# Kernel optimization log

Hardware: AMD Instinct MI355X
Metric: run time of the kernel (lower is better)

The kernel has to match this reference:

```python
import jax, jax.numpy as jnp
import numpy as np

V = 1024      # visible_size (channel_size)
H = 2048      # hidden_size
F = V + H     # full_size
T = 64        # timesteps
REC = 0.8     # params['lambda']


def setup_inputs() -> dict:
    key = jax.random.key(0)
    k1, k2, k3 = jax.random.split(key, 3)
    X = jax.random.normal(k1, (T, V), jnp.float32)
    # scale W so tanh does not fully saturate (fan-in scaling, like default init)
    W = jax.random.normal(k2, (F, F), jnp.float32) / np.float32(np.sqrt(F))
    b = jax.random.normal(k3, (F,), jnp.float32) * 0.01
    # Lambda: visible block = REC, hidden block = 1, diagonal of visible block = 1
    lam = jnp.concatenate(
        [jnp.full((V, V), REC, jnp.float32), jnp.ones((V, H), jnp.float32)], axis=1
    )
    lam = lam.at[jnp.arange(V), jnp.arange(V)].set(1.0)
    return {"X": X, "W": W, "b": b, "lam": lam}


def reference(X, W, b, lam):
    v = lam.shape[0]           # visible size
    one_minus_lam_vis = 1.0 - lam[:, :v]  # zero outside visible block anyway

    def step(carry, x_t):
        R, _ = carry
        WR = R @ W.T + b                      # [V, F] Linear applied row-wise
        U = lam * WR                          # gated recurrent part
        # I has x_t broadcast across rows in the visible block, zeros elsewhere
        U = U.at[:, :v].add(one_minus_lam_vis * x_t[None, :])
        R_next = jnp.tanh(U)                  # phi = torch.tanh
        return (R_next, U), None

    R0 = jnp.zeros((v, W.shape[0]), X.dtype)
    (_, U_last), _ = jax.lax.scan(step, (R0, R0), X)
    # torch.diag(U[:, :visible]) -> diagonal entries, shape [V]
    idx = jnp.arange(v)
    return U_last[idx, idx]
```

## Files before the change

kernel.cpp:

```cpp
#include <hip/hip_runtime.h>
#include <math.h>

#define V 1024
#define H 2048
#define F 3072
#define T 64
#define REC 0.8f

#define BM 128
#define BN 128
#define KT16 (F / 16)
#define KTW  (KT16 / 4)

typedef _Float16 half8 __attribute__((ext_vector_type(8)));
typedef float floatx16 __attribute__((ext_vector_type(16)));

__device__ __forceinline__ float fast_tanh(float u) {
    float e = __expf(2.f * u);
    return 1.f - 2.f * __builtin_amdgcn_rcpf(e + 1.f);
}


__global__ __launch_bounds__(256)
void conv_w_fm(const float* __restrict__ W, _Float16* __restrict__ Wfm) {
    const int ct = blockIdx.y;
    const int ix = blockIdx.x * 256 + threadIdx.x;
    const int kt = ix >> 8;
    const int q  = ix & 255;
    const int n  = ct * 128 + ((q >> 6) & 3) * 32 + (q & 31);
    const int k0 = kt * 16 + ((q >> 5) & 1) * 8;
    const float* src = W + (size_t)n * F + k0;
    float4 v0 = *(const float4*)src;
    float4 v1 = *(const float4*)(src + 4);
    half8 o = { (_Float16)v0.x, (_Float16)v0.y, (_Float16)v0.z, (_Float16)v0.w,
                (_Float16)v1.x, (_Float16)v1.y, (_Float16)v1.z, (_Float16)v1.w };
    *(half8*)(Wfm + ((size_t)(ct * KT16 + kt) * 2048 + q * 8)) = o;
}

__global__ __launch_bounds__(256)
void init_step0(const float* __restrict__ b, const float* __restrict__ x0,
                _Float16* __restrict__ Rfm) {
    const int rt = blockIdx.y;
    const int ix = blockIdx.x * 256 + threadIdx.x;
    const int kt = ix >> 8;
    const int q  = ix & 255;
    const int gi = rt * 128 + ((q >> 6) & 3) * 32 + (q & 31);
    const int k0 = kt * 16 + ((q >> 5) & 1) * 8;
    half8 o;
    #pragma unroll
    for (int e = 0; e < 8; ++e) {
        int gj = k0 + e;
        float wr = b[gj];
        float u = (gj >= V || gi == gj) ? wr : (REC * wr + (1.f - REC) * x0[gj]);
        o[e] = (_Float16)fast_tanh(u);
    }
    *(half8*)(Rfm + ((size_t)(rt * KT16 + kt) * 2048 + q * 8)) = o;
}

__global__ __launch_bounds__(512, 2)
void frnn_step(const _Float16* __restrict__ Rin, const _Float16* __restrict__ Wfm,
               const float* __restrict__ b, const float* __restrict__ xt,
               _Float16* __restrict__ Rout, float* __restrict__ out, int is_last)
{
    __shared__ float red[16384];

    const int tid  = threadIdx.x;
    const int lane = tid & 63;
    const int wid  = tid >> 6;
    const int sp   = wid & 1;
    const int kg   = wid >> 1;
    const int row0 = blockIdx.y * BM;
    const int col0 = blockIdx.x * BN;
    const int lane8 = lane * 8;
    const int kg48 = kg * KTW;

    const _Float16* abase = Rin + ((size_t)blockIdx.y * KT16 * 2048
                                   + sp * 1024 + lane8);
    const _Float16* bbase = Wfm + ((size_t)blockIdx.x * KT16 * 2048 + lane8);

    floatx16 acc[2][4];
    #pragma unroll
    for (int i = 0; i < 2; ++i)
        #pragma unroll
        for (int j = 0; j < 4; ++j)
            #pragma unroll
            for (int r = 0; r < 16; ++r) acc[i][j][r] = 0.f;

    half8 fa0[3], fa1[3], fb0[3], fb1[3], fb2[3], fb3[3];

#define LOADK(S, KTI)                                                           \
  {                                                                             \
    const size_t off = (size_t)(kg48 + (KTI)) * 2048;                           \
    const _Float16* ap = abase + off;                                           \
    const _Float16* bp = bbase + off;                                           \
    fa0[S] = *(const half8*)ap;                                                 \
    fa1[S] = *(const half8*)(ap + 512);                                         \
    fb0[S] = *(const half8*)bp;                                                 \
    fb1[S] = *(const half8*)(bp + 512);                                         \
    fb2[S] = *(const half8*)(bp + 1024);                                        \
    fb3[S] = *(const half8*)(bp + 1536);                                        \
  }

    LOADK(0, 0)
    LOADK(1, 1)

#define BODY(S, PFS, JJ)                                                        \
  {                                                                             \
    int pj = (JJ) + 2; if (pj > KTW - 1) pj = KTW - 1;                          \
    LOADK(PFS, pj)                                                              \
    __builtin_amdgcn_s_setprio(1);                                              \
    acc[0][0] = __builtin_amdgcn_mfma_f32_32x32x16_f16(fa0[S], fb0[S], acc[0][0],0,0,0);\
    acc[0][1] = __builtin_amdgcn_mfma_f32_32x32x16_f16(fa0[S], fb1[S], acc[0][1],0,0,0);\
    acc[0][2] = __builtin_amdgcn_mfma_f32_32x32x16_f16(fa0[S], fb2[S], acc[0][2],0,0,0);\
    acc[0][3] = __builtin_amdgcn_mfma_f32_32x32x16_f16(fa0[S], fb3[S], acc[0][3],0,0,0);\
    acc[1][0] = __builtin_amdgcn_mfma_f32_32x32x16_f16(fa1[S], fb0[S], acc[1][0],0,0,0);\
    acc[1][1] = __builtin_amdgcn_mfma_f32_32x32x16_f16(fa1[S], fb1[S], acc[1][1],0,0,0);\
    acc[1][2] = __builtin_amdgcn_mfma_f32_32x32x16_f16(fa1[S], fb2[S], acc[1][2],0,0,0);\
    acc[1][3] = __builtin_amdgcn_mfma_f32_32x32x16_f16(fa1[S], fb3[S], acc[1][3],0,0,0);\
    __builtin_amdgcn_s_setprio(0);                                              \
  }

    #pragma unroll 1
    for (int j3 = 0; j3 < KTW / 3; ++j3) {
        const int JJ = j3 * 3;
        BODY(0, 2, JJ)
        BODY(1, 0, JJ + 1)
        BODY(2, 1, JJ + 2)
    }
#undef BODY
#undef LOADK

    const int m32 = lane & 31, hh = lane >> 5;
    float b_r[4], x_r[4];
    if (kg == 0) {
        #pragma unroll
        for (int j = 0; j < 4; ++j) {
            int gj = col0 + j * 32 + m32;
            b_r[j] = b[gj];
            x_r[j] = (gj < V) ? xt[gj] : 0.f;
        }
    }

    float* red0 = &red[sp * 8192];
    float* red1 = &red[sp * 8192 + 4096];
    #pragma unroll 1
    for (int w = 1; w < 4; ++w) {
        if (kg == w) {
            #pragma unroll
            for (int j = 0; j < 4; ++j)
                #pragma unroll
                for (int q4 = 0; q4 < 4; ++q4) {
                    float4 v0 = { acc[0][j][4*q4],   acc[0][j][4*q4+1],
                                  acc[0][j][4*q4+2], acc[0][j][4*q4+3] };
                    float4 v1 = { acc[1][j][4*q4],   acc[1][j][4*q4+1],
                                  acc[1][j][4*q4+2], acc[1][j][4*q4+3] };
                    *(float4*)(red0 + (j*4 + q4) * 256 + lane * 4) = v0;
                    *(float4*)(red1 + (j*4 + q4) * 256 + lane * 4) = v1;
                }
        }
        __syncthreads();
        if (kg == 0) {
            #pragma unroll
            for (int j = 0; j < 4; ++j)
                #pragma unroll
                for (int q4 = 0; q4 < 4; ++q4) {
                    float4 v0 = *(const float4*)(red0 + (j*4 + q4) * 256 + lane * 4);
                    float4 v1 = *(const float4*)(red1 + (j*4 + q4) * 256 + lane * 4);
                    acc[0][j][4*q4]   += v0.x; acc[0][j][4*q4+1] += v0.y;
                    acc[0][j][4*q4+2] += v0.z; acc[0][j][4*q4+3] += v0.w;
                    acc[1][j][4*q4]   += v1.x; acc[1][j][4*q4+1] += v1.y;
                    acc[1][j][4*q4+2] += v1.z; acc[1][j][4*q4+3] += v1.w;
                }
        }
        __syncthreads();
    }

    if (kg == 0) {
        #pragma unroll
        for (int i = 0; i < 2; ++i) {
            const int mb = sp * 2 + i;
            #pragma unroll
            for (int j = 0; j < 4; ++j) {
                const int gj = col0 + j * 32 + m32;
                const int kt = gj >> 4;
                const int h2 = (gj >> 3) & 1;
                const int e  = gj & 7;
                _Float16* tb = Rout + ((size_t)(blockIdx.y * KT16 + kt) * 2048
                                       + (mb * 2 + h2) * 256 + e);
                const float bj = b_r[j];
                const float xj = x_r[j];
                const bool vis = (gj < V);
                #pragma unroll
                for (int r = 0; r < 16; ++r) {
                    const int mrow = 4 * hh + (r & 3) + 8 * (r >> 2);
                    const int gi = row0 + mb * 32 + mrow;
                    float wr = acc[i][j][r] + bj;
                    float u = (!vis || gi == gj) ? wr : (REC * wr + (1.f - REC) * xj);
                    tb[mrow * 8] = (_Float16)fast_tanh(u);
                    if (is_last && gi == gj) out[gi] = u;
                }
            }
        }
    }
}

extern "C" void kernel_launch(void* const* d_in, const int* in_sizes, int n_in,
                              void* d_out, int out_size, void* d_ws, size_t ws_size,
                              hipStream_t stream) {
    const float* X = (const float*)d_in[0];
    const float* W = (const float*)d_in[1];
    const float* b = (const float*)d_in[2];
    float* out = (float*)d_out;

    _Float16* Wfm = (_Float16*)d_ws;
    _Float16* Ra  = Wfm + (size_t)F * F;
    _Float16* Rb  = Ra + (size_t)V * F;

    conv_w_fm<<<dim3(192, 24), 256, 0, stream>>>(W, Wfm);
    init_step0<<<dim3(192, 8), 256, 0, stream>>>(b, X, Ra);

    for (int t = 1; t < T; ++t) {
        _Float16* Rin  = (t & 1) ? Ra : Rb;
        _Float16* Rout = (t & 1) ? Rb : Ra;
        frnn_step<<<dim3(24, 8), 512, 0, stream>>>(Rin, Wfm, b, X + (size_t)t * V,
                                                   Rout, out, t == T - 1);
    }
}
```

Measured before the change: 2.333 ms.

## Fuse per-timestep launches into persistent cooperative kernel with grid barrier

Replaces the 63 separate per-step kernel launches with one cooperative persistent kernel. The kernel loops over timesteps and synchronises all 192 blocks through an atomic counter barrier in workspace. The recurrent-state loads and stores become inline asm with cache-bypass (sc0 sc1 nt) bits so each block sees the other blocks' writes across the barrier, and explicit vmcnt waits plus sched barriers pin the prefetch pipeline. This removes launch gaps and tail effects, but adds a spin barrier and uncached traffic for R.

```diff
diff --git a/kernel.cpp b/kernel.cpp
--- a/kernel.cpp
+++ b/kernel.cpp
@@ -11,6 +11,7 @@
 #define BN 128
 #define KT16 (F / 16)
 #define KTW  (KT16 / 4)
+#define NBLK 192
 
 typedef _Float16 half8 __attribute__((ext_vector_type(8)));
 typedef float floatx16 __attribute__((ext_vector_type(16)));
@@ -39,7 +40,11 @@
 
 __global__ __launch_bounds__(256)
 void init_step0(const float* __restrict__ b, const float* __restrict__ x0,
-                _Float16* __restrict__ Rfm) {
+                _Float16* __restrict__ Rfm, unsigned* __restrict__ bar) {
+    if (blockIdx.x == 0 && blockIdx.y == 0 && threadIdx.x == 0) {
+        bar[0] = 0u;
+        bar[1] = 0u;
+    }
     const int rt = blockIdx.y;
     const int ix = blockIdx.x * 256 + threadIdx.x;
     const int kt = ix >> 8;
@@ -58,9 +63,10 @@
 }
 
 __global__ __launch_bounds__(512, 2)
-void frnn_step(const _Float16* __restrict__ Rin, const _Float16* __restrict__ Wfm,
-               const float* __restrict__ b, const float* __restrict__ xt,
-               _Float16* __restrict__ Rout, float* __restrict__ out, int is_last)
+void frnn_persist(const _Float16* __restrict__ Wfm, _Float16* __restrict__ Ra,
+                  _Float16* __restrict__ Rb, const float* __restrict__ b,
+                  const float* __restrict__ X, float* __restrict__ out,
+                  unsigned* __restrict__ bar)
 {
     __shared__ float red[16384];
 
@@ -73,41 +79,55 @@
     const int col0 = blockIdx.x * BN;
     const int lane8 = lane * 8;
     const int kg48 = kg * KTW;
-
-    const _Float16* abase = Rin + ((size_t)blockIdx.y * KT16 * 2048
-                                   + sp * 1024 + lane8);
+    const int m32 = lane & 31, hh = lane >> 5;
+
     const _Float16* bbase = Wfm + ((size_t)blockIdx.x * KT16 * 2048 + lane8);
 
-    floatx16 acc[2][4];
-    #pragma unroll
-    for (int i = 0; i < 2; ++i)
+    half8 fa0[3], fa1[3], fb0[3], fb1[3], fb2[3], fb3[3];
+
+    #pragma unroll 1
+    for (int t = 1; t < T; ++t) {
+        const _Float16* Rin  = (t & 1) ? Ra : Rb;
+        _Float16*       Rout = (t & 1) ? Rb : Ra;
+        const float*    xt   = X + (size_t)t * V;
+        const _Float16* abase = Rin + ((size_t)blockIdx.y * KT16 * 2048
+                                       + sp * 1024 + lane8);
+
+        floatx16 acc[2][4];
         #pragma unroll
-        for (int j = 0; j < 4; ++j)
+        for (int i = 0; i < 2; ++i)
             #pragma unroll
-            for (int r = 0; r < 16; ++r) acc[i][j][r] = 0.f;
-
-    half8 fa0[3], fa1[3], fb0[3], fb1[3], fb2[3], fb3[3];
+            for (int j = 0; j < 4; ++j)
+                #pragma unroll
+                for (int r = 0; r < 16; ++r) acc[i][j][r] = 0.f;
 
 #define LOADK(S, KTI)                                                           \
   {                                                                             \
     const size_t off = (size_t)(kg48 + (KTI)) * 2048;                           \
     const _Float16* ap = abase + off;                                           \
     const _Float16* bp = bbase + off;                                           \
-    fa0[S] = *(const half8*)ap;                                                 \
-    fa1[S] = *(const half8*)(ap + 512);                                         \
-    fb0[S] = *(const half8*)bp;                                                 \
-    fb1[S] = *(const half8*)(bp + 512);                                         \
-    fb2[S] = *(const half8*)(bp + 1024);                                        \
-    fb3[S] = *(const half8*)(bp + 1536);                                        \
+    asm volatile("global_load_dwordx4 %0, %2, off sc0 sc1 nt\n\t"               \
+                 "global_load_dwordx4 %1, %3, off sc0 sc1 nt"                   \
+                 : "=&v"(fa0[S]), "=&v"(fa1[S])                                 \
+                 : "v"(ap), "v"(ap + 512));                                     \
+    asm volatile("global_load_dwordx4 %0, %4, off\n\t"                          \
+                 "global_load_dwordx4 %1, %5, off\n\t"                          \
+                 "global_load_dwordx4 %2, %6, off\n\t"                          \
+                 "global_load_dwordx4 %3, %7, off"                              \
+                 : "=&v"(fb0[S]), "=&v"(fb1[S]), "=&v"(fb2[S]), "=&v"(fb3[S])   \
+                 : "v"(bp), "v"(bp + 512), "v"(bp + 1024), "v"(bp + 1536));     \
   }
 
-    LOADK(0, 0)
-    LOADK(1, 1)
+        LOADK(0, 0)
+        LOADK(1, 1)
 
 #define BODY(S, PFS, JJ)                                                        \
   {                                                                             \
+    asm volatile("s_waitcnt vmcnt(6)" ::: "memory");                            \
+    __builtin_amdgcn_sched_barrier(0);                                          \
     int pj = (JJ) + 2; if (pj > KTW - 1) pj = KTW - 1;                          \
     LOADK(PFS, pj)                                                              \
+    __builtin_amdgcn_sched_barrier(0);                                          \
     __builtin_amdgcn_s_setprio(1);                                              \
     acc[0][0] = __builtin_amdgcn_mfma_f32_32x32x16_f16(fa0[S], fb0[S], acc[0][0],0,0,0);\
     acc[0][1] = __builtin_amdgcn_mfma_f32_32x32x16_f16(fa0[S], fb1[S], acc[0][1],0,0,0);\
@@ -120,86 +140,109 @@
     __builtin_amdgcn_s_setprio(0);                                              \
   }
 
-    #pragma unroll 1
-    for (int j3 = 0; j3 < KTW / 3; ++j3) {
-        const int JJ = j3 * 3;
-        BODY(0, 2, JJ)
-        BODY(1, 0, JJ + 1)
-        BODY(2, 1, JJ + 2)
-    }
+        #pragma unroll 1
+        for (int j3 = 0; j3 < KTW / 3; ++j3) {
+            const int JJ = j3 * 3;
+            BODY(0, 2, JJ)
+            BODY(1, 0, JJ + 1)
+            BODY(2, 1, JJ + 2)
+        }
 #undef BODY
 #undef LOADK
 
-    const int m32 = lane & 31, hh = lane >> 5;
-    float b_r[4], x_r[4];
-    if (kg == 0) {
-        #pragma unroll
-        for (int j = 0; j < 4; ++j) {
-            int gj = col0 + j * 32 + m32;
-            b_r[j] = b[gj];
-            x_r[j] = (gj < V) ? xt[gj] : 0.f;
-        }
-    }
-
-    float* red0 = &red[sp * 8192];
-    float* red1 = &red[sp * 8192 + 4096];
-    #pragma unroll 1
-    for (int w = 1; w < 4; ++w) {
-        if (kg == w) {
-            #pragma unroll
-            for (int j = 0; j < 4; ++j)
-                #pragma unroll
-                for (int q4 = 0; q4 < 4; ++q4) {
-                    float4 v0 = { acc[0][j][4*q4],   acc[0][j][4*q4+1],
-                                  acc[0][j][4*q4+2], acc[0][j][4*q4+3] };
-                    float4 v1 = { acc[1][j][4*q4],   acc[1][j][4*q4+1],
-                                  acc[1][j][4*q4+2], acc[1][j][4*q4+3] };
-                    *(float4*)(red0 + (j*4 + q4) * 256 + lane * 4) = v0;
-                    *(float4*)(red1 + (j*4 + q4) * 256 + lane * 4) = v1;
-                }
-        }
-        __syncthreads();
+        asm volatile("s_waitcnt vmcnt(0)" ::: "memory");
+
+        float b_r[4], x_r[4];
         if (kg == 0) {
             #pragma unroll
-            for (int j = 0; j < 4; ++j)
-                #pragma unroll
-                for (int q4 = 0; q4 < 4; ++q4) {
-                    float4 v0 = *(const float4*)(red0 + (j*4 + q4) * 256 + lane * 4);
-                    float4 v1 = *(const float4*)(red1 + (j*4 + q4) * 256 + lane * 4);
-                    acc[0][j][4*q4]   += v0.x; acc[0][j][4*q4+1] += v0.y;
-                    acc[0][j][4*q4+2] += v0.z; acc[0][j][4*q4+3] += v0.w;
-                    acc[1][j][4*q4]   += v1.x; acc[1][j][4*q4+1] += v1.y;
-                    acc[1][j][4*q4+2] += v1.z; acc[1][j][4*q4+3] += v1.w;
+            for (int j = 0; j < 4; ++j) {
+                int gj = col0 + j * 32 + m32;
+                b_r[j] = b[gj];
+                x_r[j] = (gj < V) ? xt[gj] : 0.f;
+            }
+        }
+
+        float* red0 = &red[sp * 8192];
+        float* red1 = &red[sp * 8192 + 4096];
+        #pragma unroll 1
+        for (int w = 1; w < 4; ++w) {
+            if (kg == w) {
+                #pragma unroll
+                for (int j = 0; j < 4; ++j)
+                    #pragma unroll
+                    for (int q4 = 0; q4 < 4; ++q4) {
+                        float4 v0 = { acc[0][j][4*q4],   acc[0][j][4*q4+1],
+                                      acc[0][j][4*q4+2], acc[0][j][4*q4+3] };
+                        float4 v1 = { acc[1][j][4*q4],   acc[1][j][4*q4+1],
+                                      acc[1][j][4*q4+2], acc[1][j][4*q4+3] };
+                        *(float4*)(red0 + (j*4 + q4) * 256 + lane * 4) = v0;
+                        *(float4*)(red1 + (j*4 + q4) * 256 + lane * 4) = v1;
+                    }
+            }
+            __syncthreads();
+            if (kg == 0) {
+                #pragma unroll
+                for (int j = 0; j < 4; ++j)
+                    #pragma unroll
+                    for (int q4 = 0; q4 < 4; ++q4) {
+                        float4 v0 = *(const float4*)(red0 + (j*4 + q4) * 256 + lane * 4);
+                        float4 v1 = *(const float4*)(red1 + (j*4 + q4) * 256 + lane * 4);
+                        acc[0][j][4*q4]   += v0.x; acc[0][j][4*q4+1] += v0.y;
+                        acc[0][j][4*q4+2] += v0.z; acc[0][j][4*q4+3] += v0.w;
+                        acc[1][j][4*q4]   += v1.x; acc[1][j][4*q4+1] += v1.y;
+                        acc[1][j][4*q4+2] += v1.z; acc[1][j][4*q4+3] += v1.w;
+                    }
+            }
+            __syncthreads();
+        }
+
+        if (kg == 0) {
+            #pragma unroll
+            for (int i = 0; i < 2; ++i) {
+                const int mb = sp * 2 + i;
+                #pragma unroll
+                for (int j = 0; j < 4; ++j) {
+                    const int gj = col0 + j * 32 + m32;
+                    const int kt = gj >> 4;
+                    const int h2 = (gj >> 3) & 1;
+                    const int e  = gj & 7;
+                    _Float16* tb = Rout + ((size_t)(blockIdx.y * KT16 + kt) * 2048
+                                           + (mb * 2 + h2) * 256 + e);
+                    const float bj = b_r[j];
+                    const float xj = x_r[j];
+                    const bool vis = (gj < V);
+                    #pragma unroll
+                    for (int r = 0; r < 16; ++r) {
+                        const int mrow = 4 * hh + (r & 3) + 8 * (r >> 2);
+                        const int gi = row0 + mb * 32 + mrow;
+                        float wr = acc[i][j][r] + bj;
+                        float u = (!vis || gi == gj) ? wr : (REC * wr + (1.f - REC) * xj);
+                        _Float16 rv = (_Float16)fast_tanh(u);
+                        asm volatile("global_store_short %0, %1, off sc0 sc1 nt"
+                                     :: "v"(tb + mrow * 8), "v"(rv) : "memory");
+                        if ((t == T - 1) && (gi == gj)) out[gi] = u;
+                    }
                 }
-        }
-        __syncthreads();
-    }
-
-    if (kg == 0) {
-        #pragma unroll
-        for (int i = 0; i < 2; ++i) {
-            const int mb = sp * 2 + i;
-            #pragma unroll
-            for (int j = 0; j < 4; ++j) {
-                const int gj = col0 + j * 32 + m32;
-                const int kt = gj >> 4;
-                const int h2 = (gj >> 3) & 1;
-                const int e  = gj & 7;
-                _Float16* tb = Rout + ((size_t)(blockIdx.y * KT16 + kt) * 2048
-                                       + (mb * 2 + h2) * 256 + e);
-                const float bj = b_r[j];
-                const float xj = x_r[j];
-                const bool vis = (gj < V);
-                #pragma unroll
-                for (int r = 0; r < 16; ++r) {
-                    const int mrow = 4 * hh + (r & 3) + 8 * (r >> 2);
-                    const int gi = row0 + mb * 32 + mrow;
-                    float wr = acc[i][j][r] + bj;
-                    float u = (!vis || gi == gj) ? wr : (REC * wr + (1.f - REC) * xj);
-                    tb[mrow * 8] = (_Float16)fast_tanh(u);
-                    if (is_last && gi == gj) out[gi] = u;
+            }
+        }
+
+        if (t < T - 1) {
+            __syncthreads();
+            asm volatile("s_waitcnt vmcnt(0)" ::: "memory");
+            __syncthreads();
+            if (tid == 0) {
+                unsigned arr = __hip_atomic_fetch_add(&bar[0], 1u,
+                                   __ATOMIC_RELAXED, __HIP_MEMORY_SCOPE_AGENT) + 1u;
+                if (arr == (unsigned)(t * NBLK)) {
+                    __hip_atomic_store(&bar[1], (unsigned)t,
+                                       __ATOMIC_RELAXED, __HIP_MEMORY_SCOPE_AGENT);
+                } else {
+                    while (__hip_atomic_load(&bar[1], __ATOMIC_RELAXED,
+                                             __HIP_MEMORY_SCOPE_AGENT) < (unsigned)t)
+                        __builtin_amdgcn_s_sleep(2);
                 }
             }
+            __syncthreads();
         }
     }
 }
@@ -215,14 +258,19 @@
     _Float16* Wfm = (_Float16*)d_ws;
     _Float16* Ra  = Wfm + (size_t)F * F;
     _Float16* Rb  = Ra + (size_t)V * F;
+    unsigned* bar = (unsigned*)(Rb + (size_t)V * F);
 
     conv_w_fm<<<dim3(192, 24), 256, 0, stream>>>(W, Wfm);
-    init_step0<<<dim3(192, 8), 256, 0, stream>>>(b, X, Ra);
-
-    for (int t = 1; t < T; ++t) {
-        _Float16* Rin  = (t & 1) ? Ra : Rb;
-        _Float16* Rout = (t & 1) ? Rb : Ra;
-        frnn_step<<<dim3(24, 8), 512, 0, stream>>>(Rin, Wfm, b, X + (size_t)t * V,
-                                                   Rout, out, t == T - 1);
-    }
-}
+    init_step0<<<dim3(192, 8), 256, 0, stream>>>(b, X, Ra, bar);
+
+    const _Float16* WfmP = Wfm;
+    _Float16* RaP = Ra;
+    _Float16* RbP = Rb;
+    const float* bP = b;
+    const float* XP = X;
+    float* outP = out;
+    unsigned* barP = bar;
+    void* kargs[] = { &WfmP, &RaP, &RbP, &bP, &XP, &outP, &barP };
+    (void)hipLaunchCooperativeKernel((void*)frnn_persist, dim3(24, 8), dim3(512),
+                                     kargs, 0, stream);
+}
```

After: 4.350 ms. 1.86x slower.
